# Kernel optimization log

Hardware: AMD Instinct MI355X
Metric: run time of the kernel (lower is better)

The kernel has to match this reference:

```python
import jax, jax.numpy as jnp
import numpy as np

HID = 10
IN_DIM = 256
B, H, W = 8, 96, 96


def _conv(x, w, b=None, pad=0):
    y = jax.lax.conv_general_dilated(x, w, (1, 1), [(pad, pad), (pad, pad)],
                                     dimension_numbers=('NCHW', 'OIHW', 'NCHW'))
    return y if b is None else y + b[None, :, None, None]


def _bn(x, g, b):
    # eval-mode InPlaceABN(Sync) with identity running stats -> per-channel affine
    return x * g[None, :, None, None] + b[None, :, None, None]


def _branch(x, w1, g1, b1, w2, g2, b2):
    # Conv3x3 -> BN -> ReLU -> Conv1x1 -> BN -> ReLU  (relation / comp_u / comp_l)
    y = jax.nn.relu(_bn(_conv(x, w1, pad=1), g1, b1))
    return jax.nn.relu(_bn(_conv(y, w2), g2, b2))


def _gru(x, h, gw, gb, cw, cg, cb):
    # ConvGRU with 1x1 kernels
    gates = _conv(jnp.concatenate([x, h], axis=1), gw, gb)
    r = jax.nn.sigmoid(gates[:, 0:1])
    u = jax.nn.sigmoid(gates[:, 1:2])
    cnm = jax.nn.relu(_bn(_conv(jnp.concatenate([x, r * h], axis=1), cw), cg, cb))
    return (1.0 - u) * h + u * cnm


def setup_inputs():
    key = jax.random.key(0)
    ks = iter(jax.random.split(key, 48))

    def nrm(shape, s=0.05):
        return jax.random.normal(next(ks), shape, jnp.float32) * s

    inp = {
        'f_nodes': jax.random.normal(next(ks), (2, B, HID, H, W), jnp.float32),
        'h_nodes': jax.random.normal(next(ks), (3, B, HID, H, W), jnp.float32),
        'p_nodes': jax.random.normal(next(ks), (7, B, HID, H, W), jnp.float32),
        'xh': jax.random.normal(next(ks), (B, IN_DIM, H, W), jnp.float32),
        'f_atts': jax.random.uniform(next(ks), (2, B, 1, H, W), jnp.float32),
        'p_atts': jax.random.uniform(next(ks), (7, B, 1, H, W), jnp.float32),
        # Decomposition.decomp_att: Conv3x3(257->256)+BN+ReLU, Conv1x1(256->2)+bias
        'da_w1': nrm((IN_DIM, IN_DIM + 1, 3, 3)),
        'da_g1': jnp.ones((IN_DIM,), jnp.float32),
        'da_b1': jnp.zeros((IN_DIM,), jnp.float32),
        'da_w2': nrm((2, IN_DIM, 1, 1)),
        'da_b2': jnp.zeros((2,), jnp.float32),
    }
    # relation (shared across children), comp_u, comp_l: Conv3x3(20->10)+BN+ReLU, Conv1x1(10->10)+BN+ReLU
    for p in ('rel', 'cu', 'cl'):
        inp[p + '_w1'] = nrm((HID, 2 * HID, 3, 3))
        inp[p + '_g1'] = jnp.ones((HID,), jnp.float32)
        inp[p + '_b1'] = jnp.zeros((HID,), jnp.float32)
        inp[p + '_w2'] = nrm((HID, HID, 1, 1))
        inp[p + '_g2'] = jnp.ones((HID,), jnp.float32)
        inp[p + '_b2'] = jnp.zeros((HID,), jnp.float32)
    # 3 ConvGRUs (cls_h), 1x1 kernels, stacked on leading dim
    inp['gru_gw'] = nrm((3, 2, 2 * HID, 1, 1))
    inp['gru_gb'] = jnp.zeros((3, 2), jnp.float32)
    inp['gru_cw'] = nrm((3, HID, 2 * HID, 1, 1))
    inp['gru_cg'] = jnp.ones((3, HID), jnp.float32)
    inp['gru_cb'] = jnp.zeros((3, HID), jnp.float32)
    return inp


def reference(f_nodes, h_nodes, p_nodes, xh, f_atts, p_atts,
              da_w1, da_g1, da_b1, da_w2, da_b2,
              rel_w1, rel_g1, rel_b1, rel_w2, rel_g2, rel_b2,
              cu_w1, cu_g1, cu_b1, cu_w2, cu_g2, cu_b2,
              cl_w1, cl_g1, cl_b1, cl_w2, cl_g2, cl_b2,
              gru_gw, gru_gb, gru_cw, gru_cg, gru_cb):
    parent, parent_att = f_nodes[1], f_atts[1]
    # Decomposition of full-body node into 2 half nodes
    dm = _conv(jnp.concatenate([parent_att, xh], axis=1), da_w1, pad=1)
    dm = jax.nn.relu(_bn(dm, da_g1, da_b1))
    dm = _conv(dm, da_w2, da_b2)  # [B, 2, H, W] decomposition map
    datt = jax.nn.softmax(dm, axis=1)
    decomp = [_branch(jnp.concatenate([parent * datt[:, i:i + 1] * parent_att,
                                       h_nodes[1 + i]], axis=1),
                      rel_w1, rel_g1, rel_b1, rel_w2, rel_g2, rel_b2)
              for i in range(2)]
    # node 0: background
    n0 = _gru(f_nodes[0] + p_nodes[0], h_nodes[0],
              gru_gw[0], gru_gb[0], gru_cw[0], gru_cg[0], gru_cb[0])
    # node 1: upper half = composition(upper parts 1-4) + decomposition
    up = jnp.sum(p_nodes[1:5], axis=0) * jnp.sum(p_atts[1:5], axis=0)
    comp_u = _branch(jnp.concatenate([h_nodes[1], up], axis=1),
                     cu_w1, cu_g1, cu_b1, cu_w2, cu_g2, cu_b2)
    n1 = _gru(comp_u + decomp[0], h_nodes[1],
              gru_gw[1], gru_gb[1], gru_cw[1], gru_cg[1], gru_cb[1])
    # node 2: lower half = composition(lower parts 5-6) + decomposition
    lo = jnp.sum(p_nodes[5:7], axis=0) * jnp.sum(p_atts[5:7], axis=0)
    comp_l = _branch(jnp.concatenate([h_nodes[2], lo], axis=1),
                     cl_w1, cl_g1, cl_b1, cl_w2, cl_g2, cl_b2)
    n2 = _gru(comp_l + decomp[1], h_nodes[2],
              gru_gw[2], gru_gb[2], gru_cw[2], gru_cg[2], gru_cb[2])
    return (jnp.stack([n0, n1, n2]), dm)
```

## Files before the change

kernel.cpp:

```cpp
#include <hip/hip_runtime.h>
#include <cstddef>
#include <cstdint>

constexpr int Bn    = 8;
constexpr int Hn    = 96;
constexpr int Wn    = 96;
constexpr int HWn   = Hn * Wn;
constexpr int BHWn  = Bn * HWn;
constexpr int B10HW = Bn * 10 * HWn;

using short8  = __attribute__((ext_vector_type(8))) short;
using ushort8 = __attribute__((ext_vector_type(8))) unsigned short;
using float4v = __attribute__((ext_vector_type(4))) float;

__device__ __forceinline__ unsigned short f2bf(float f) {
    unsigned u = __builtin_bit_cast(unsigned, f);
    u += 0x7FFFu + ((u >> 16) & 1u);
    return (unsigned short)(u >> 16);
}

__global__ void k_packw(const float* __restrict__ w1, short* __restrict__ wpk)
{
    const int idx = blockIdx.x * 256 + threadIdx.x;
    if (idx >= 82944) return;
    const int lane = idx & 63;
    const int q    = (idx >> 6) & 15;
    const int ct   = idx >> 10;
    const int tap  = ct % 9;
    const int cb   = ct / 9;
    const int co   = q * 16 + (lane & 15);
    const int ci0  = cb * 32 + ((lane >> 4) * 8);
    ushort8 v;
    #pragma unroll
    for (int j = 0; j < 8; ++j) {
        const int ci = ci0 + j;
        const float f = (ci < 257) ? w1[((size_t)co * 257 + ci) * 9 + tap] : 0.f;
        v[j] = f2bf(f);
    }
    *(ushort8*)(wpk + (size_t)idx * 8) = v;
}

__global__ __launch_bounds__(256)
void k_bigconv_mfma(const float* __restrict__ xh, const float* __restrict__ patt,
                    const short* __restrict__ wpk, const float* __restrict__ g1,
                    const float* __restrict__ b1, const float* __restrict__ w2,
                    float* __restrict__ dm_acc)
{
    __shared__ __align__(16) short xs[4 * 204 * 8];

    const int tid    = threadIdx.x;
    const int lane   = tid & 63;
    const int wid    = tid >> 6;
    const int wave_m = wid >> 1;
    const int wave_n = wid & 1;
    const int bx     = blockIdx.x;
    const int wseg   = bx % 3;
    const int hb     = (bx / 3) % 24;
    const int b      = bx / 72;
    const int h0     = hb * 4, w0 = wseg * 32;
    const int am     = lane & 15;
    const int aq     = lane >> 4;
    const int qbase  = blockIdx.y * 8 + wave_n * 4;

    float4v acc[4][4];
    #pragma unroll
    for (int i = 0; i < 4; ++i)
        #pragma unroll
        for (int j = 0; j < 4; ++j)
            acc[i][j] = float4v{0.f, 0.f, 0.f, 0.f};

    int arow[4], acol[4];
    #pragma unroll
    for (int mt = 0; mt < 4; ++mt) {
        const int m = wave_m * 64 + mt * 16 + am;
        arow[mt] = m >> 5;
        acol[mt] = m & 31;
    }

    for (int cb = 0; cb < 9; ++cb) {
        __syncthreads();
        {
            const int g    = wid;
            const int cig0 = cb * 32 + g * 8;
            for (int pos = lane; pos < 204; pos += 64) {
                const int row = pos / 34, col = pos % 34;
                const int hh = h0 - 1 + row, ww = w0 - 1 + col;
                const bool inb = ((unsigned)hh < (unsigned)Hn) & ((unsigned)ww < (unsigned)Wn);
                const int off = hh * Wn + ww;
                ushort8 v;
                #pragma unroll
                for (int j = 0; j < 8; ++j) {
                    const int ci = cig0 + j;
                    float f = 0.f;
                    if (inb && ci < 257)
                        f = (ci == 0) ? patt[b * HWn + off]
                                      : xh[((size_t)b * 256 + (ci - 1)) * HWn + off];
                    v[j] = f2bf(f);
                }
                *(ushort8*)&xs[(g * 204 + pos) * 8] = v;
            }
        }
        __syncthreads();

        const short* wb = wpk + (((size_t)cb * 9) * 16 * 64) * 8;
        for (int tap = 0; tap < 9; ++tap) {
            const int kh = tap / 3, kw = tap % 3;
            short8 bfr[4];
            const short* wt = wb + ((size_t)tap * 16 * 64) * 8;
            #pragma unroll
            for (int nt = 0; nt < 4; ++nt)
                bfr[nt] = *(const short8*)(wt + ((size_t)(qbase + nt) * 64 + lane) * 8);
            short8 afr[4];
            #pragma unroll
            for (int mt = 0; mt < 4; ++mt) {
                const int pos = (arow[mt] + kh) * 34 + (acol[mt] + kw);
                afr[mt] = *(const short8*)&xs[(aq * 204 + pos) * 8];
            }
            #pragma unroll
            for (int mt = 0; mt < 4; ++mt)
                #pragma unroll
                for (int nt = 0; nt < 4; ++nt)
                    acc[mt][nt] = __builtin_amdgcn_mfma_f32_16x16x32_bf16(
                        afr[mt], bfr[nt], acc[mt][nt], 0, 0, 0);
        }
    }

    float gv[4], bv[4], wa[4], wbv[4];
    const int ncol = blockIdx.y * 128 + wave_n * 64 + am;
    #pragma unroll
    for (int nt = 0; nt < 4; ++nt) {
        const int co = ncol + nt * 16;
        gv[nt]  = g1[co];
        bv[nt]  = b1[co];
        wa[nt]  = w2[co];
        wbv[nt] = w2[256 + co];
    }
    #pragma unroll
    for (int mt = 0; mt < 4; ++mt) {
        #pragma unroll
        for (int reg = 0; reg < 4; ++reg) {
            float s0 = 0.f, s1 = 0.f;
            #pragma unroll
            for (int nt = 0; nt < 4; ++nt) {
                const float y = fmaxf(fmaf(acc[mt][nt][reg], gv[nt], bv[nt]), 0.f);
                s0 = fmaf(wa[nt], y, s0);
                s1 = fmaf(wbv[nt], y, s1);
            }
            #pragma unroll
            for (int off = 1; off < 16; off <<= 1) {
                s0 += __shfl_xor(s0, off, 64);
                s1 += __shfl_xor(s1, off, 64);
            }
            if (am == 0) {
                const int m = wave_m * 64 + mt * 16 + aq * 4 + reg;
                const int r = m >> 5, c = m & 31;
                const size_t o = (size_t)(b * 2) * HWn + (h0 + r) * Wn + (w0 + c);
                atomicAdd(&dm_acc[o], s0);
                atomicAdd(&dm_acc[o + HWn], s1);
            }
        }
    }
}

__global__ void k_dm_soft(const float* __restrict__ dm_acc, const float* __restrict__ db2,
                          const float* __restrict__ patt, float* __restrict__ dm_out,
                          float* __restrict__ s01)
{
    const int p = blockIdx.x * 256 + threadIdx.x;
    if (p >= BHWn) return;
    const int b = p / HWn, hw = p % HWn;
    const size_t i0 = (size_t)(b * 2) * HWn + hw;
    const size_t i1 = (size_t)(b * 2 + 1) * HWn + hw;
    float d0 = dm_acc[i0] + db2[0];
    float d1 = dm_acc[i1] + db2[1];
    dm_out[i0] = d0;
    dm_out[i1] = d1;
    float m  = fmaxf(d0, d1);
    float e0 = expf(d0 - m), e1 = expf(d1 - m);
    float pa = patt[p];
    float inv = pa / (e0 + e1);
    s01[p]        = e0 * inv;
    s01[BHWn + p] = e1 * inv;
}

__global__ void k_uplo(const float* __restrict__ pn, const float* __restrict__ pa,
                       float* __restrict__ up, float* __restrict__ lo)
{
    const int p = blockIdx.x * 256 + threadIdx.x;
    if (p >= BHWn) return;
    const int b = p / HWn, hw = p % HWn;
    float au = 0.f, al = 0.f;
    for (int k = 1; k <= 4; ++k) au += pa[(size_t)(k * Bn + b) * HWn + hw];
    for (int k = 5; k <= 6; ++k) al += pa[(size_t)(k * Bn + b) * HWn + hw];
    for (int c = 0; c < 10; ++c) {
        float su = 0.f, sl = 0.f;
        for (int k = 1; k <= 4; ++k) su += pn[((size_t)(k * Bn + b) * 10 + c) * HWn + hw];
        for (int k = 5; k <= 6; ++k) sl += pn[((size_t)(k * Bn + b) * 10 + c) * HWn + hw];
        up[((size_t)b * 10 + c) * HWn + hw] = su * au;
        lo[((size_t)b * 10 + c) * HWn + hw] = sl * al;
    }
}

struct BranchW  { const float *w1, *g1, *b1, *w2, *g2, *b2; };
struct BranchW3 { BranchW p[3]; };

__global__ __launch_bounds__(256)
void k_branch(BranchW3 P, const float* __restrict__ parent, const float* __restrict__ h_nodes,
              const float* __restrict__ s01, const float* __restrict__ up,
              const float* __restrict__ lo, float* __restrict__ bout)
{
    const int z  = blockIdx.z;
    const int pi = (z < 2) ? 0 : (z - 1);
    __shared__ float wl[1800], w2l[100], g1l[10], b1l[10], g2l[10], b2l[10];
    const BranchW& Pw = P.p[pi];
    for (int i = threadIdx.x; i < 1800; i += 256) wl[i] = Pw.w1[i];
    if (threadIdx.x < 100) w2l[threadIdx.x] = Pw.w2[threadIdx.x];
    if (threadIdx.x < 10) {
        g1l[threadIdx.x] = Pw.g1[threadIdx.x];
        b1l[threadIdx.x] = Pw.b1[threadIdx.x];
        g2l[threadIdx.x] = Pw.g2[threadIdx.x];
        b2l[threadIdx.x] = Pw.b2[threadIdx.x];
    }
    __syncthreads();

    const int p = blockIdx.x * 256 + threadIdx.x;
    const int b = p / HWn, hw = p % HWn, h = hw / Wn, w = hw % Wn;

    const float* Ab = nullptr;
    const float* sc = nullptr;
    const float* Bb = nullptr;
    if (z == 0)      { Ab = parent; sc = s01;        Bb = h_nodes + (size_t)1 * B10HW; }
    else if (z == 1) { Ab = parent; sc = s01 + BHWn; Bb = h_nodes + (size_t)2 * B10HW; }
    else if (z == 2) { Ab = h_nodes + (size_t)1 * B10HW; Bb = up; }
    else             { Ab = h_nodes + (size_t)2 * B10HW; Bb = lo; }

    float acc[10] = {};
    for (int kh = 0; kh < 3; ++kh) {
        const int hh = h + kh - 1;
        if ((unsigned)hh >= (unsigned)Hn) continue;
        for (int kw = 0; kw < 3; ++kw) {
            const int ww = w + kw - 1;
            if ((unsigned)ww >= (unsigned)Wn) continue;
            const int off = hh * Wn + ww;
            const int tap = kh * 3 + kw;
            const float scv = sc ? sc[b * HWn + off] : 1.f;
            #pragma unroll
            for (int ci = 0; ci < 20; ++ci) {
                float v;
                if (ci < 10) v = Ab[((size_t)b * 10 + ci) * HWn + off] * scv;
                else         v = Bb[((size_t)b * 10 + (ci - 10)) * HWn + off];
                #pragma unroll
                for (int co = 0; co < 10; ++co)
                    acc[co] = fmaf(wl[(co * 20 + ci) * 9 + tap], v, acc[co]);
            }
        }
    }
    float y[10];
    #pragma unroll
    for (int co = 0; co < 10; ++co)
        y[co] = fmaxf(fmaf(acc[co], g1l[co], b1l[co]), 0.f);
    #pragma unroll
    for (int co = 0; co < 10; ++co) {
        float s = 0.f;
        #pragma unroll
        for (int i = 0; i < 10; ++i) s = fmaf(w2l[co * 10 + i], y[i], s);
        s = fmaxf(fmaf(s, g2l[co], b2l[co]), 0.f);
        bout[(size_t)z * B10HW + ((size_t)b * 10 + co) * HWn + hw] = s;
    }
}

__global__ void k_gru(const float* __restrict__ f_nodes, const float* __restrict__ h_nodes,
                      const float* __restrict__ p_nodes, const float* __restrict__ bout,
                      const float* __restrict__ gw, const float* __restrict__ gb,
                      const float* __restrict__ cw, const float* __restrict__ cg,
                      const float* __restrict__ cb, float* __restrict__ out)
{
    const int z = blockIdx.y;
    __shared__ float gwl[40], cwl[200], gbl[2], cgl[10], cbl[10];
    if (threadIdx.x < 40)  gwl[threadIdx.x] = gw[z * 40 + threadIdx.x];
    if (threadIdx.x < 200) cwl[threadIdx.x] = cw[z * 200 + threadIdx.x];
    if (threadIdx.x < 2)   gbl[threadIdx.x] = gb[z * 2 + threadIdx.x];
    if (threadIdx.x < 10) {
        cgl[threadIdx.x] = cg[z * 10 + threadIdx.x];
        cbl[threadIdx.x] = cb[z * 10 + threadIdx.x];
    }
    __syncthreads();

    const int p = blockIdx.x * 256 + threadIdx.x;
    const int b = p / HWn, hw = p % HWn;
    float x[10], h[10];
    #pragma unroll
    for (int c = 0; c < 10; ++c) {
        const size_t idx = ((size_t)b * 10 + c) * HWn + hw;
        if (z == 0)      x[c] = f_nodes[idx] + p_nodes[idx];
        else if (z == 1) x[c] = bout[(size_t)2 * B10HW + idx] + bout[idx];
        else             x[c] = bout[(size_t)3 * B10HW + idx] + bout[(size_t)1 * B10HW + idx];
        h[c] = h_nodes[(size_t)z * B10HW + idx];
    }
    float g0 = gbl[0], g1 = gbl[1];
    #pragma unroll
    for (int c = 0; c < 10; ++c) {
        g0 = fmaf(gwl[c],      x[c], g0);
        g0 = fmaf(gwl[10 + c], h[c], g0);
        g1 = fmaf(gwl[20 + c], x[c], g1);
        g1 = fmaf(gwl[30 + c], h[c], g1);
    }
    const float r = 1.f / (1.f + expf(-g0));
    const float u = 1.f / (1.f + expf(-g1));
    #pragma unroll
    for (int o = 0; o < 10; ++o) {
        float s = 0.f;
        #pragma unroll
        for (int c = 0; c < 10; ++c) {
            s = fmaf(cwl[o * 20 + c],      x[c],     s);
            s = fmaf(cwl[o * 20 + 10 + c], r * h[c], s);
        }
        s = fmaxf(fmaf(s, cgl[o], cbl[o]), 0.f);
        out[(size_t)z * B10HW + ((size_t)b * 10 + o) * HWn + hw] =
            (1.f - u) * h[o] + u * s;
    }
}

extern "C" void kernel_launch(void* const* d_in, const int* in_sizes, int n_in,
                              void* d_out, int out_size, void* d_ws, size_t ws_size,
                              hipStream_t stream)
{
    (void)in_sizes; (void)n_in; (void)out_size; (void)ws_size;

    const float* f_nodes = (const float*)d_in[0];
    const float* h_nodes = (const float*)d_in[1];
    const float* p_nodes = (const float*)d_in[2];
    const float* xh      = (const float*)d_in[3];
    const float* f_atts  = (const float*)d_in[4];
    const float* p_atts  = (const float*)d_in[5];
    const float* da_w1   = (const float*)d_in[6];
    const float* da_g1   = (const float*)d_in[7];
    const float* da_b1   = (const float*)d_in[8];
    const float* da_w2   = (const float*)d_in[9];
    const float* da_b2   = (const float*)d_in[10];

    BranchW3 P;
    for (int i = 0; i < 3; ++i) {
        P.p[i].w1 = (const float*)d_in[11 + 6 * i + 0];
        P.p[i].g1 = (const float*)d_in[11 + 6 * i + 1];
        P.p[i].b1 = (const float*)d_in[11 + 6 * i + 2];
        P.p[i].w2 = (const float*)d_in[11 + 6 * i + 3];
        P.p[i].g2 = (const float*)d_in[11 + 6 * i + 4];
        P.p[i].b2 = (const float*)d_in[11 + 6 * i + 5];
    }
    const float* gru_gw = (const float*)d_in[29];
    const float* gru_gb = (const float*)d_in[30];
    const float* gru_cw = (const float*)d_in[31];
    const float* gru_cg = (const float*)d_in[32];
    const float* gru_cb = (const float*)d_in[33];

    float* out    = (float*)d_out;
    float* dm_out = out + (size_t)3 * B10HW;

    float* ws     = (float*)d_ws;
    float* dm_acc = ws;
    float* s01    = dm_acc + 2 * BHWn;
    float* up     = s01 + 2 * BHWn;
    float* lo     = up + B10HW;
    float* bout   = lo + B10HW;
    short* wpk    = (short*)s01;

    const float* patt   = f_atts + BHWn;
    const float* parent = f_nodes + B10HW;

    hipMemsetAsync(dm_acc, 0, (size_t)2 * BHWn * sizeof(float), stream);
    k_packw<<<dim3(324), 256, 0, stream>>>(da_w1, wpk);
    k_bigconv_mfma<<<dim3(576, 2), 256, 0, stream>>>(xh, patt, wpk, da_g1, da_b1,
                                                     da_w2, dm_acc);
    k_dm_soft<<<dim3(288), 256, 0, stream>>>(dm_acc, da_b2, patt, dm_out, s01);
    k_uplo<<<dim3(288), 256, 0, stream>>>(p_nodes, p_atts, up, lo);
    k_branch<<<dim3(288, 1, 4), 256, 0, stream>>>(P, parent, h_nodes, s01, up, lo, bout);
    k_gru<<<dim3(288, 3), 256, 0, stream>>>(f_nodes, h_nodes, p_nodes, bout,
                                            gru_gw, gru_gb, gru_cw, gru_cg, gru_cb, out);
}
```

Before: 436.5 us.

## Fuse softmax into double-buffered full-N MFMA conv and tile branch conv via LDS

The big 3x3 conv now has each block compute all 256 output channels (so no atomics), double-buffers the LDS input tile and prefetches weights one tap ahead. The 1x1 reduction, softmax and attention scaling are fused into its epilogue, which removes the memset and the separate softmax kernel. The small branch conv is rewritten to stage a halo tile and transposed, padded weights in LDS and use float4 weight loads. The risks are more accumulator registers per thread (acc[4][8]), half as many blocks for the big conv, and wpk now aliasing the bout workspace.

```diff
diff --git a/kernel.cpp b/kernel.cpp
--- a/kernel.cpp
+++ b/kernel.cpp
@@ -25,9 +25,9 @@
     if (idx >= 82944) return;
     const int lane = idx & 63;
     const int q    = (idx >> 6) & 15;
-    const int ct   = idx >> 10;
-    const int tap  = ct % 9;
-    const int cb   = ct / 9;
+    const int t    = idx >> 10;
+    const int tap  = t % 9;
+    const int cb   = t / 9;
     const int co   = q * 16 + (lane & 15);
     const int ci0  = cb * 32 + ((lane >> 4) * 8);
     ushort8 v;
@@ -40,13 +40,15 @@
     *(ushort8*)(wpk + (size_t)idx * 8) = v;
 }
 
-__global__ __launch_bounds__(256)
-void k_bigconv_mfma(const float* __restrict__ xh, const float* __restrict__ patt,
-                    const short* __restrict__ wpk, const float* __restrict__ g1,
-                    const float* __restrict__ b1, const float* __restrict__ w2,
-                    float* __restrict__ dm_acc)
-{
-    __shared__ __align__(16) short xs[4 * 204 * 8];
+__global__ __launch_bounds__(256, 2)
+void k_bigconv2(const float* __restrict__ xh, const float* __restrict__ patt,
+                const short* __restrict__ wpk, const float* __restrict__ g1,
+                const float* __restrict__ b1, const float* __restrict__ w2,
+                const float* __restrict__ db2,
+                float* __restrict__ dm_out, float* __restrict__ s01)
+{
+    __shared__ __align__(16) short xs[2][4][205][8];
+    __shared__ float part[2][128][2];
 
     const int tid    = threadIdx.x;
     const int lane   = tid & 63;
@@ -60,13 +62,12 @@
     const int h0     = hb * 4, w0 = wseg * 32;
     const int am     = lane & 15;
     const int aq     = lane >> 4;
-    const int qbase  = blockIdx.y * 8 + wave_n * 4;
-
-    float4v acc[4][4];
+
+    float4v acc[4][8];
     #pragma unroll
     for (int i = 0; i < 4; ++i)
         #pragma unroll
-        for (int j = 0; j < 4; ++j)
+        for (int j = 0; j < 8; ++j)
             acc[i][j] = float4v{0.f, 0.f, 0.f, 0.f};
 
     int arow[4], acol[4];
@@ -77,59 +78,70 @@
         acol[mt] = m & 31;
     }
 
+    auto stageX = [&](int cb, int buf) {
+        const int cig0 = cb * 32 + wid * 8;
+        for (int pos = lane; pos < 204; pos += 64) {
+            const int row = pos / 34, col = pos % 34;
+            const int hh = h0 - 1 + row, ww = w0 - 1 + col;
+            const bool inb = ((unsigned)hh < (unsigned)Hn) & ((unsigned)ww < (unsigned)Wn);
+            const int off = hh * Wn + ww;
+            ushort8 v;
+            #pragma unroll
+            for (int j = 0; j < 8; ++j) {
+                const int ci = cig0 + j;
+                float f = 0.f;
+                if (inb && ci < 257)
+                    f = (ci == 0) ? patt[b * HWn + off]
+                                  : xh[((size_t)b * 256 + (ci - 1)) * HWn + off];
+                v[j] = f2bf(f);
+            }
+            *(ushort8*)&xs[buf][wid][pos][0] = v;
+        }
+    };
+
+    const short8* wp = (const short8*)wpk;
+    const int qb = wave_n * 8;
+
+    stageX(0, 0);
+    short8 bfr[8], bnx[8];
+    #pragma unroll
+    for (int nt = 0; nt < 8; ++nt)
+        bfr[nt] = wp[(size_t)(qb + nt) * 64 + lane];
+    __syncthreads();
+
     for (int cb = 0; cb < 9; ++cb) {
-        __syncthreads();
-        {
-            const int g    = wid;
-            const int cig0 = cb * 32 + g * 8;
-            for (int pos = lane; pos < 204; pos += 64) {
-                const int row = pos / 34, col = pos % 34;
-                const int hh = h0 - 1 + row, ww = w0 - 1 + col;
-                const bool inb = ((unsigned)hh < (unsigned)Hn) & ((unsigned)ww < (unsigned)Wn);
-                const int off = hh * Wn + ww;
-                ushort8 v;
+        const int buf = cb & 1;
+        for (int tap = 0; tap < 9; ++tap) {
+            const int t = cb * 9 + tap;
+            if (t < 80) {
                 #pragma unroll
-                for (int j = 0; j < 8; ++j) {
-                    const int ci = cig0 + j;
-                    float f = 0.f;
-                    if (inb && ci < 257)
-                        f = (ci == 0) ? patt[b * HWn + off]
-                                      : xh[((size_t)b * 256 + (ci - 1)) * HWn + off];
-                    v[j] = f2bf(f);
-                }
-                *(ushort8*)&xs[(g * 204 + pos) * 8] = v;
-            }
-        }
-        __syncthreads();
-
-        const short* wb = wpk + (((size_t)cb * 9) * 16 * 64) * 8;
-        for (int tap = 0; tap < 9; ++tap) {
+                for (int nt = 0; nt < 8; ++nt)
+                    bnx[nt] = wp[((size_t)(t + 1) * 16 + qb + nt) * 64 + lane];
+            }
             const int kh = tap / 3, kw = tap % 3;
-            short8 bfr[4];
-            const short* wt = wb + ((size_t)tap * 16 * 64) * 8;
-            #pragma unroll
-            for (int nt = 0; nt < 4; ++nt)
-                bfr[nt] = *(const short8*)(wt + ((size_t)(qbase + nt) * 64 + lane) * 8);
             short8 afr[4];
             #pragma unroll
             for (int mt = 0; mt < 4; ++mt) {
                 const int pos = (arow[mt] + kh) * 34 + (acol[mt] + kw);
-                afr[mt] = *(const short8*)&xs[(aq * 204 + pos) * 8];
+                afr[mt] = *(const short8*)&xs[buf][aq][pos][0];
             }
             #pragma unroll
             for (int mt = 0; mt < 4; ++mt)
                 #pragma unroll
-                for (int nt = 0; nt < 4; ++nt)
+                for (int nt = 0; nt < 8; ++nt)
                     acc[mt][nt] = __builtin_amdgcn_mfma_f32_16x16x32_bf16(
                         afr[mt], bfr[nt], acc[mt][nt], 0, 0, 0);
-        }
-    }
-
-    float gv[4], bv[4], wa[4], wbv[4];
-    const int ncol = blockIdx.y * 128 + wave_n * 64 + am;
-    #pragma unroll
-    for (int nt = 0; nt < 4; ++nt) {
-        const int co = ncol + nt * 16;
+            #pragma unroll
+            for (int nt = 0; nt < 8; ++nt) bfr[nt] = bnx[nt];
+        }
+        if (cb < 8) stageX(cb + 1, buf ^ 1);
+        __syncthreads();
+    }
+
+    float gv[8], bv[8], wa[8], wbv[8];
+    #pragma unroll
+    for (int nt = 0; nt < 8; ++nt) {
+        const int co = wave_n * 128 + nt * 16 + am;
         gv[nt]  = g1[co];
         bv[nt]  = b1[co];
         wa[nt]  = w2[co];
@@ -141,7 +153,7 @@
         for (int reg = 0; reg < 4; ++reg) {
             float s0 = 0.f, s1 = 0.f;
             #pragma unroll
-            for (int nt = 0; nt < 4; ++nt) {
+            for (int nt = 0; nt < 8; ++nt) {
                 const float y = fmaxf(fmaf(acc[mt][nt][reg], gv[nt], bv[nt]), 0.f);
                 s0 = fmaf(wa[nt], y, s0);
                 s1 = fmaf(wbv[nt], y, s1);
@@ -153,34 +165,26 @@
             }
             if (am == 0) {
                 const int m = wave_m * 64 + mt * 16 + aq * 4 + reg;
-                const int r = m >> 5, c = m & 31;
-                const size_t o = (size_t)(b * 2) * HWn + (h0 + r) * Wn + (w0 + c);
-                atomicAdd(&dm_acc[o], s0);
-                atomicAdd(&dm_acc[o + HWn], s1);
-            }
-        }
-    }
-}
-
-__global__ void k_dm_soft(const float* __restrict__ dm_acc, const float* __restrict__ db2,
-                          const float* __restrict__ patt, float* __restrict__ dm_out,
-                          float* __restrict__ s01)
-{
-    const int p = blockIdx.x * 256 + threadIdx.x;
-    if (p >= BHWn) return;
-    const int b = p / HWn, hw = p % HWn;
-    const size_t i0 = (size_t)(b * 2) * HWn + hw;
-    const size_t i1 = (size_t)(b * 2 + 1) * HWn + hw;
-    float d0 = dm_acc[i0] + db2[0];
-    float d1 = dm_acc[i1] + db2[1];
-    dm_out[i0] = d0;
-    dm_out[i1] = d1;
-    float m  = fmaxf(d0, d1);
-    float e0 = expf(d0 - m), e1 = expf(d1 - m);
-    float pa = patt[p];
-    float inv = pa / (e0 + e1);
-    s01[p]        = e0 * inv;
-    s01[BHWn + p] = e1 * inv;
+                part[wave_n][m][0] = s0;
+                part[wave_n][m][1] = s1;
+            }
+        }
+    }
+    __syncthreads();
+    if (tid < 128) {
+        const int m = tid, r = m >> 5, c = m & 31;
+        const int off = (h0 + r) * Wn + (w0 + c);
+        float d0 = part[0][m][0] + part[1][m][0] + db2[0];
+        float d1 = part[0][m][1] + part[1][m][1] + db2[1];
+        dm_out[(size_t)(b * 2) * HWn + off]     = d0;
+        dm_out[(size_t)(b * 2 + 1) * HWn + off] = d1;
+        const float mx = fmaxf(d0, d1);
+        const float e0 = expf(d0 - mx), e1 = expf(d1 - mx);
+        const float pa = patt[b * HWn + off];
+        const float inv = pa / (e0 + e1);
+        s01[b * HWn + off]        = e0 * inv;
+        s01[BHWn + b * HWn + off] = e1 * inv;
+    }
 }
 
 __global__ void k_uplo(const float* __restrict__ pn, const float* __restrict__ pa,
@@ -209,56 +213,77 @@
               const float* __restrict__ s01, const float* __restrict__ up,
               const float* __restrict__ lo, float* __restrict__ bout)
 {
-    const int z  = blockIdx.z;
+    const int z  = blockIdx.y;
     const int pi = (z < 2) ? 0 : (z - 1);
-    __shared__ float wl[1800], w2l[100], g1l[10], b1l[10], g2l[10], b2l[10];
+    __shared__ float xt[20][10][34];
+    __shared__ __align__(16) float wlt[9 * 20 * 12];
+    __shared__ float w2l[100], g1l[10], b1l[10], g2l[10], b2l[10];
+
     const BranchW& Pw = P.p[pi];
-    for (int i = threadIdx.x; i < 1800; i += 256) wl[i] = Pw.w1[i];
-    if (threadIdx.x < 100) w2l[threadIdx.x] = Pw.w2[threadIdx.x];
-    if (threadIdx.x < 10) {
-        g1l[threadIdx.x] = Pw.g1[threadIdx.x];
-        b1l[threadIdx.x] = Pw.b1[threadIdx.x];
-        g2l[threadIdx.x] = Pw.g2[threadIdx.x];
-        b2l[threadIdx.x] = Pw.b2[threadIdx.x];
-    }
-    __syncthreads();
-
-    const int p = blockIdx.x * 256 + threadIdx.x;
-    const int b = p / HWn, hw = p % HWn, h = hw / Wn, w = hw % Wn;
-
-    const float* Ab = nullptr;
+    const int tid = threadIdx.x;
+    for (int idx = tid; idx < 2160; idx += 256) {
+        const int co = idx % 12, rem = idx / 12, ci = rem % 20, tap = rem / 20;
+        wlt[idx] = (co < 10) ? Pw.w1[(co * 20 + ci) * 9 + tap] : 0.f;
+    }
+    if (tid < 100) w2l[tid] = Pw.w2[tid];
+    if (tid < 10) {
+        g1l[tid] = Pw.g1[tid]; b1l[tid] = Pw.b1[tid];
+        g2l[tid] = Pw.g2[tid]; b2l[tid] = Pw.b2[tid];
+    }
+
+    const int bx = blockIdx.x;
+    const int tw = bx % 3, th = (bx / 3) % 12, b = bx / 36;
+    const int h0 = th * 8, w0 = tw * 32;
+
+    const float* Ab;
     const float* sc = nullptr;
-    const float* Bb = nullptr;
+    const float* Bb;
     if (z == 0)      { Ab = parent; sc = s01;        Bb = h_nodes + (size_t)1 * B10HW; }
     else if (z == 1) { Ab = parent; sc = s01 + BHWn; Bb = h_nodes + (size_t)2 * B10HW; }
     else if (z == 2) { Ab = h_nodes + (size_t)1 * B10HW; Bb = up; }
     else             { Ab = h_nodes + (size_t)2 * B10HW; Bb = lo; }
 
-    float acc[10] = {};
-    for (int kh = 0; kh < 3; ++kh) {
-        const int hh = h + kh - 1;
-        if ((unsigned)hh >= (unsigned)Hn) continue;
-        for (int kw = 0; kw < 3; ++kw) {
-            const int ww = w + kw - 1;
-            if ((unsigned)ww >= (unsigned)Wn) continue;
+    for (int idx = tid; idx < 6800; idx += 256) {
+        const int col = idx % 34, rem = idx / 34, row = rem % 10, ch = rem / 10;
+        const int hh = h0 - 1 + row, ww = w0 - 1 + col;
+        float v = 0.f;
+        if (((unsigned)hh < (unsigned)Hn) & ((unsigned)ww < (unsigned)Wn)) {
             const int off = hh * Wn + ww;
-            const int tap = kh * 3 + kw;
-            const float scv = sc ? sc[b * HWn + off] : 1.f;
-            #pragma unroll
-            for (int ci = 0; ci < 20; ++ci) {
-                float v;
-                if (ci < 10) v = Ab[((size_t)b * 10 + ci) * HWn + off] * scv;
-                else         v = Bb[((size_t)b * 10 + (ci - 10)) * HWn + off];
-                #pragma unroll
-                for (int co = 0; co < 10; ++co)
-                    acc[co] = fmaf(wl[(co * 20 + ci) * 9 + tap], v, acc[co]);
-            }
-        }
-    }
+            if (ch < 10) {
+                v = Ab[((size_t)b * 10 + ch) * HWn + off];
+                if (sc) v *= sc[b * HWn + off];
+            } else {
+                v = Bb[((size_t)b * 10 + (ch - 10)) * HWn + off];
+            }
+        }
+        ((float*)xt)[idx] = v;
+    }
+    __syncthreads();
+
+    const int r = tid >> 5, c = tid & 31;
+    float a0 = 0, a1 = 0, a2 = 0, a3 = 0, a4 = 0, a5 = 0, a6 = 0, a7 = 0, a8 = 0, a9 = 0;
+    #pragma unroll
+    for (int tap = 0; tap < 9; ++tap) {
+        const int kh = tap / 3, kw = tap % 3;
+        #pragma unroll
+        for (int ci = 0; ci < 20; ++ci) {
+            const float xv = xt[ci][r + kh][c + kw];
+            const float4 wA = *(const float4*)&wlt[(tap * 20 + ci) * 12];
+            const float4 wB = *(const float4*)&wlt[(tap * 20 + ci) * 12 + 4];
+            const float2 wC = *(const float2*)&wlt[(tap * 20 + ci) * 12 + 8];
+            a0 = fmaf(wA.x, xv, a0); a1 = fmaf(wA.y, xv, a1);
+            a2 = fmaf(wA.z, xv, a2); a3 = fmaf(wA.w, xv, a3);
+            a4 = fmaf(wB.x, xv, a4); a5 = fmaf(wB.y, xv, a5);
+            a6 = fmaf(wB.z, xv, a6); a7 = fmaf(wB.w, xv, a7);
+            a8 = fmaf(wC.x, xv, a8); a9 = fmaf(wC.y, xv, a9);
+        }
+    }
+    float acc[10] = {a0, a1, a2, a3, a4, a5, a6, a7, a8, a9};
     float y[10];
     #pragma unroll
     for (int co = 0; co < 10; ++co)
         y[co] = fmaxf(fmaf(acc[co], g1l[co], b1l[co]), 0.f);
+    const int hw = (h0 + r) * Wn + (w0 + c);
     #pragma unroll
     for (int co = 0; co < 10; ++co) {
         float s = 0.f;
@@ -358,23 +383,20 @@
     float* dm_out = out + (size_t)3 * B10HW;
 
     float* ws     = (float*)d_ws;
-    float* dm_acc = ws;
-    float* s01    = dm_acc + 2 * BHWn;
+    float* s01    = ws;
     float* up     = s01 + 2 * BHWn;
     float* lo     = up + B10HW;
     float* bout   = lo + B10HW;
-    short* wpk    = (short*)s01;
+    short* wpk    = (short*)bout;
 
     const float* patt   = f_atts + BHWn;
     const float* parent = f_nodes + B10HW;
 
-    hipMemsetAsync(dm_acc, 0, (size_t)2 * BHWn * sizeof(float), stream);
     k_packw<<<dim3(324), 256, 0, stream>>>(da_w1, wpk);
-    k_bigconv_mfma<<<dim3(576, 2), 256, 0, stream>>>(xh, patt, wpk, da_g1, da_b1,
-                                                     da_w2, dm_acc);
-    k_dm_soft<<<dim3(288), 256, 0, stream>>>(dm_acc, da_b2, patt, dm_out, s01);
+    k_bigconv2<<<dim3(576), 256, 0, stream>>>(xh, patt, wpk, da_g1, da_b1,
+                                              da_w2, da_b2, dm_out, s01);
     k_uplo<<<dim3(288), 256, 0, stream>>>(p_nodes, p_atts, up, lo);
-    k_branch<<<dim3(288, 1, 4), 256, 0, stream>>>(P, parent, h_nodes, s01, up, lo, bout);
+    k_branch<<<dim3(288, 4), 256, 0, stream>>>(P, parent, h_nodes, s01, up, lo, bout);
     k_gru<<<dim3(288, 3), 256, 0, stream>>>(f_nodes, h_nodes, p_nodes, bout,
                                             gru_gw, gru_gb, gru_cw, gru_cg, gru_cb, out);
 }
```

Result: faster. 407.6 us (-6.6%).
